# Kernel tuning notes

Hardware: AMD Instinct MI355X
Metric: run time of the kernel (lower is better)

Reference implementation:

```python
import jax, jax.numpy as jnp
import numpy as np

C = 512      # filters
G = 32       # groups
EPS = 1e-6

def setup_inputs() -> dict:
    key = jax.random.key(0)
    ks = jax.random.split(key, 10)
    B, H, W = 2, 64, 64
    inputs = jax.random.normal(ks[0], (B, H, W, C), dtype=jnp.float32)
    scale = 1.0 / np.sqrt(C)
    def w(k):
        return jax.random.normal(k, (C, C), dtype=jnp.float32) * scale
    return {
        "inputs": inputs,
        "gn_gamma": jnp.ones((C,), jnp.float32),
        "gn_beta": jnp.zeros((C,), jnp.float32),
        "wq": w(ks[1]), "bq": jnp.zeros((C,), jnp.float32),
        "wk": w(ks[2]), "bk": jnp.zeros((C,), jnp.float32),
        "wv": w(ks[3]), "bv": jnp.zeros((C,), jnp.float32),
        "wo": w(ks[4]), "bo": jnp.zeros((C,), jnp.float32),
    }

def _group_norm(x, gamma, beta):
    B, H, W, c = x.shape
    xg = x.reshape(B, H, W, G, c // G)
    mean = jnp.mean(xg, axis=(1, 2, 4), keepdims=True)
    var = jnp.var(xg, axis=(1, 2, 4), keepdims=True)
    xg = (xg - mean) * jax.lax.rsqrt(var + EPS)
    return xg.reshape(B, H, W, c) * gamma + beta

def reference(inputs, gn_gamma, gn_beta, wq, bq, wk, bk, wv, bv, wo, bo):
    B, H, W, c = inputs.shape
    x = _group_norm(inputs, gn_gamma, gn_beta)
    # 1x1 convs == per-pixel linear layers
    q = (x @ wq + bq).reshape(B, H * W, c)
    k = (x @ wk + bk).reshape(B, H * W, c)
    v = (x @ wv + bv).reshape(B, H * W, c)
    q = q * jnp.asarray(1.0 / np.sqrt(float(c)), q.dtype)
    scores = jnp.einsum('bnc,bmc->bnm', q, k).astype(jnp.float32)  # [B,N,N]
    probs = jax.nn.softmax(scores, axis=-1).astype(inputs.dtype)
    attn = jnp.einsum('bnm,bmc->bnc', probs, v)
    out = attn.reshape(B, H, W, c) @ wo + bo
    return out + inputs
```

## Files before the change

### kernel.cpp

```cpp
#include <hip/hip_runtime.h>
#include <math.h>

typedef __bf16 bf16;
typedef __bf16 bf16x8 __attribute__((ext_vector_type(8)));
typedef float  f32x4  __attribute__((ext_vector_type(4)));

#define DEV __device__ __forceinline__

DEV void gload_lds16(const bf16* g, bf16* l) {
  __builtin_amdgcn_global_load_lds(
      (const __attribute__((address_space(1))) void*)g,
      (__attribute__((address_space(3))) void*)l, 16, 0, 0);
}

#define OFF_STATS 0UL
#define OFF_XN    512UL
#define OFF_WTQKV 8389120UL
#define OFF_WOT   9961984UL
#define OFF_BIASQ 10486272UL
#define OFF_QKV   10492416UL
#define OFF_VT    35658240UL
#define OFF_S     44046848UL
#define OFF_ATTN  111155712UL

__global__ __launch_bounds__(256) void gn_part_k(const float* __restrict__ x,
                                                 float2* __restrict__ part) {
  const int blk = blockIdx.x;
  const int chunk = blk & 15;
  const int bg = blk >> 4;
  const int b = bg >> 5, g = bg & 31;
  const int t = threadIdx.x;
  const int p = chunk * 256 + t;
  const float* xp = x + (size_t)b * (4096 * 512) + (size_t)p * 512 + g * 16;
  float4 v0 = *(const float4*)(xp);
  float4 v1 = *(const float4*)(xp + 4);
  float4 v2 = *(const float4*)(xp + 8);
  float4 v3 = *(const float4*)(xp + 12);
  float s  = v0.x + v0.y + v0.z + v0.w + v1.x + v1.y + v1.z + v1.w
           + v2.x + v2.y + v2.z + v2.w + v3.x + v3.y + v3.z + v3.w;
  float ss = v0.x*v0.x + v0.y*v0.y + v0.z*v0.z + v0.w*v0.w
           + v1.x*v1.x + v1.y*v1.y + v1.z*v1.z + v1.w*v1.w
           + v2.x*v2.x + v2.y*v2.y + v2.z*v2.z + v2.w*v2.w
           + v3.x*v3.x + v3.y*v3.y + v3.z*v3.z + v3.w*v3.w;
#pragma unroll
  for (int off = 32; off; off >>= 1) {
    s  += __shfl_xor(s, off);
    ss += __shfl_xor(ss, off);
  }
  __shared__ float rs[4], rss[4];
  const int w = t >> 6, l = t & 63;
  if (l == 0) { rs[w] = s; rss[w] = ss; }
  __syncthreads();
  if (t == 0)
    part[blk] = make_float2(rs[0] + rs[1] + rs[2] + rs[3],
                            rss[0] + rss[1] + rss[2] + rss[3]);
}

__global__ void gn_finish_k(const float2* __restrict__ part,
                            float2* __restrict__ stats) {
  const int g = threadIdx.x;
  float s = 0.f, ss = 0.f;
#pragma unroll
  for (int c = 0; c < 16; ++c) {
    float2 p = part[g * 16 + c];
    s += p.x; ss += p.y;
  }
  float mean = s * (1.0f / 65536.0f);
  float var  = ss * (1.0f / 65536.0f) - mean * mean;
  stats[g] = make_float2(mean, 1.0f / sqrtf(var + 1e-6f));
}

__global__ __launch_bounds__(256) void gn_apply_k(const float* __restrict__ x,
                                                  const float2* __restrict__ stats,
                                                  const float* __restrict__ gamma,
                                                  const float* __restrict__ beta,
                                                  bf16* __restrict__ xn) {
  size_t i = ((size_t)blockIdx.x * 256 + threadIdx.x) * 8;
  const int c = (int)(i & 511);
  const int b = (int)(i >> 21);
  float2 st = stats[b * 32 + (c >> 4)];
  float4 xa = *(const float4*)(x + i);
  float4 xb = *(const float4*)(x + i + 4);
  float4 ga = *(const float4*)(gamma + c);
  float4 gb = *(const float4*)(gamma + c + 4);
  float4 ba = *(const float4*)(beta + c);
  float4 bb = *(const float4*)(beta + c + 4);
  bf16x8 o;
  o[0] = (bf16)((xa.x - st.x) * st.y * ga.x + ba.x);
  o[1] = (bf16)((xa.y - st.x) * st.y * ga.y + ba.y);
  o[2] = (bf16)((xa.z - st.x) * st.y * ga.z + ba.z);
  o[3] = (bf16)((xa.w - st.x) * st.y * ga.w + ba.w);
  o[4] = (bf16)((xb.x - st.x) * st.y * gb.x + bb.x);
  o[5] = (bf16)((xb.y - st.x) * st.y * gb.y + bb.y);
  o[6] = (bf16)((xb.z - st.x) * st.y * gb.z + bb.z);
  o[7] = (bf16)((xb.w - st.x) * st.y * gb.w + bb.w);
  *(bf16x8*)(xn + i) = o;
}

__global__ void prep_w_k(const float* __restrict__ wq, const float* __restrict__ wk,
                         const float* __restrict__ wv, const float* __restrict__ wo,
                         bf16* __restrict__ wt_qkv, bf16* __restrict__ wot, float qscale) {
  const int z = blockIdx.z;
  const float* W = (z == 0) ? wq : (z == 1) ? wk : (z == 2) ? wv : wo;
  bf16* dst = (z < 3) ? (wt_qkv + (size_t)z * 512 * 512) : wot;
  const float s = (z == 0) ? qscale : 1.0f;
  __shared__ float tile[32][33];
  const int i0 = blockIdx.y * 32;
  const int o0 = blockIdx.x * 32;
#pragma unroll
  for (int r = threadIdx.y; r < 32; r += 8)
    tile[r][threadIdx.x] = W[(size_t)(i0 + r) * 512 + o0 + threadIdx.x];
  __syncthreads();
#pragma unroll
  for (int r = threadIdx.y; r < 32; r += 8)
    dst[(size_t)(o0 + r) * 512 + i0 + threadIdx.x] = (bf16)(tile[threadIdx.x][r] * s);
}

__global__ void prep_bias_k(const float* __restrict__ bq, const float* __restrict__ bk,
                            const float* __restrict__ bv, float* __restrict__ bias_qkv,
                            float qscale) {
  int i = blockIdx.x * 256 + threadIdx.x;
  float v = (i < 512) ? bq[i] * qscale : (i < 1024) ? bk[i - 512] : bv[i - 1024];
  bias_qkv[i] = v;
}

__global__ void transpose_v_k(const bf16* __restrict__ qkv, bf16* __restrict__ vt) {
  __shared__ bf16 tile[32][33];
  const int z = blockIdx.z;
  const int n0 = blockIdx.x * 32, d0 = blockIdx.y * 32;
  const bf16* src = qkv + (size_t)z * 4096 * 1536 + 1024;
#pragma unroll
  for (int r = threadIdx.y; r < 32; r += 8)
    tile[r][threadIdx.x] = src[(size_t)(n0 + r) * 1536 + d0 + threadIdx.x];
  __syncthreads();
  bf16* dst = vt + (size_t)z * 512 * 4096;
#pragma unroll
  for (int r = threadIdx.y; r < 32; r += 8)
    dst[(size_t)(d0 + r) * 4096 + n0 + threadIdx.x] = tile[threadIdx.x][r];
}

__global__ __launch_bounds__(256) void softmax_k(bf16* __restrict__ S) {
  const int t = threadIdx.x;
  bf16* p = S + (size_t)blockIdx.x * 4096 + t * 16;
  bf16x8 u0 = *(const bf16x8*)p;
  bf16x8 u1 = *(const bf16x8*)(p + 8);
  float v[16];
#pragma unroll
  for (int j = 0; j < 8; ++j) { v[j] = (float)u0[j]; v[j + 8] = (float)u1[j]; }
  float m = v[0];
#pragma unroll
  for (int j = 1; j < 16; ++j) m = fmaxf(m, v[j]);
#pragma unroll
  for (int off = 32; off; off >>= 1) m = fmaxf(m, __shfl_xor(m, off));
  __shared__ float red[4];
  const int w = t >> 6, l = t & 63;
  if (l == 0) red[w] = m;
  __syncthreads();
  m = fmaxf(fmaxf(red[0], red[1]), fmaxf(red[2], red[3]));
  __syncthreads();
  float s = 0.f;
#pragma unroll
  for (int j = 0; j < 16; ++j) { v[j] = __expf(v[j] - m); s += v[j]; }
#pragma unroll
  for (int off = 32; off; off >>= 1) s += __shfl_xor(s, off);
  if (l == 0) red[w] = s;
  __syncthreads();
  s = red[0] + red[1] + red[2] + red[3];
  const float inv = 1.0f / s;
#pragma unroll
  for (int j = 0; j < 8; ++j) { u0[j] = (bf16)(v[j] * inv); u1[j] = (bf16)(v[j + 8] * inv); }
  *(bf16x8*)p = u0;
  *(bf16x8*)(p + 8) = u1;
}

template <int BM, int BN, int EPI, int GX, int GY, int GZ>
__global__ __launch_bounds__(256, 2) void gemm_nt(
    const bf16* __restrict__ A, int lda, long sAz,
    const bf16* __restrict__ B, int ldb, long sBz,
    void* __restrict__ C, int ldc, long sCz,
    int nk,
    const float* __restrict__ bias,
    const float* __restrict__ resid) {
  constexpr int WM = BM / 2, WN = BN / 2;
  constexpr int FM = BM / 32, FN = BN / 32;
  constexpr int NWG = GX * GY * GZ;
  constexpr int CPX = NWG / 8;
  __shared__ alignas(16) bf16 As[2][BM * 64];
  __shared__ alignas(16) bf16 Bs[2][BN * 64];

  const int lin = blockIdx.x;
  const int wid = (lin & 7) * CPX + (lin >> 3);
  const int bx = wid % GX;
  const int by = (wid / GX) % GY;
  const int bz = wid / (GX * GY);

  const int t = threadIdx.x;
  const bf16* Aq = A + (size_t)bz * sAz + (size_t)by * BM * lda;
  const bf16* Bq = B + (size_t)bz * sBz + (size_t)bx * BN * ldb;

  const int srow = t >> 3;
  const int sg   = (t & 7) ^ (srow & 7);

  auto stage = [&](int buf, int kt) {
    const int k0 = kt * 64 + sg * 8;
#pragma unroll
    for (int i = 0; i < BM / 32; ++i)
      gload_lds16(Aq + (size_t)(i * 32 + srow) * lda + k0, &As[buf][i * 2048 + t * 8]);
#pragma unroll
    for (int i = 0; i < BN / 32; ++i)
      gload_lds16(Bq + (size_t)(i * 32 + srow) * ldb + k0, &Bs[buf][i * 2048 + t * 8]);
  };

  const int l = t & 63, w = t >> 6;
  const int wr = w >> 1, wc = w & 1;
  const int lr = l & 15, kh = l >> 4;
  const int rs = lr & 7;

  f32x4 acc[FM][FN] = {};

  stage(0, 0);
  for (int kt = 0; kt < nk; ++kt) {
    __syncthreads();
    if (kt + 1 < nk) stage((kt + 1) & 1, kt + 1);
    const int buf = kt & 1;
    bf16x8 a[2][FM], b[2][FN];
#pragma unroll
    for (int h = 0; h < 2; ++h) {
      const int g = ((h * 4 + kh) ^ rs) * 8;
#pragma unroll
      for (int m = 0; m < FM; ++m)
        a[h][m] = *(const bf16x8*)(&As[buf][(wr * WM + m * 16 + lr) * 64 + g]);
#pragma unroll
      for (int n = 0; n < FN; ++n)
        b[h][n] = *(const bf16x8*)(&Bs[buf][(wc * WN + n * 16 + lr) * 64 + g]);
    }
#pragma unroll
    for (int h = 0; h < 2; ++h)
#pragma unroll
      for (int m = 0; m < FM; ++m)
#pragma unroll
        for (int n = 0; n < FN; ++n)
          acc[m][n] = __builtin_amdgcn_mfma_f32_16x16x32_bf16(a[h][m], b[h][n], acc[m][n], 0, 0, 0);
  }

  const int gr0 = by * BM + wr * WM + kh * 4;
  const int gc0 = bx * BN + wc * WN + lr;
#pragma unroll
  for (int m = 0; m < FM; ++m)
#pragma unroll
    for (int n = 0; n < FN; ++n) {
      const int c = gc0 + n * 16;
      float bv = 0.f;
      if constexpr (EPI >= 1) bv = bias[c];
#pragma unroll
      for (int j = 0; j < 4; ++j) {
        const int r = gr0 + m * 16 + j;
        float val = acc[m][n][j] + bv;
        if constexpr (EPI == 2) {
          float* Cf = (float*)C + (size_t)bz * sCz;
          Cf[(size_t)r * ldc + c] = val + resid[(size_t)r * ldc + c];
        } else {
          bf16* Cb = (bf16*)C + (size_t)bz * sCz;
          Cb[(size_t)r * ldc + c] = (bf16)val;
        }
      }
    }
}

extern "C" void kernel_launch(void* const* d_in, const int* in_sizes, int n_in,
                              void* d_out, int out_size, void* d_ws, size_t ws_size,
                              hipStream_t stream) {
  const float* x     = (const float*)d_in[0];
  const float* gamma = (const float*)d_in[1];
  const float* beta  = (const float*)d_in[2];
  const float* wq = (const float*)d_in[3];
  const float* bq = (const float*)d_in[4];
  const float* wk = (const float*)d_in[5];
  const float* bk = (const float*)d_in[6];
  const float* wv = (const float*)d_in[7];
  const float* bv = (const float*)d_in[8];
  const float* wo = (const float*)d_in[9];
  const float* bo = (const float*)d_in[10];
  float* out = (float*)d_out;
  char* ws = (char*)d_ws;

  float2* stats    = (float2*)(ws + OFF_STATS);
  bf16*   xn       = (bf16*)(ws + OFF_XN);
  bf16*   wt_qkv   = (bf16*)(ws + OFF_WTQKV);
  bf16*   wot      = (bf16*)(ws + OFF_WOT);
  float*  bias_qkv = (float*)(ws + OFF_BIASQ);
  bf16*   qkv      = (bf16*)(ws + OFF_QKV);
  bf16*   vt       = (bf16*)(ws + OFF_VT);
  bf16*   S        = (bf16*)(ws + OFF_S);
  bf16*   attn     = (bf16*)(ws + OFF_ATTN);
  float2* gn_part  = (float2*)(ws + OFF_S);

  const float qscale = 0.04419417382415922f;

  prep_w_k<<<dim3(16, 16, 4), dim3(32, 8), 0, stream>>>(wq, wk, wv, wo, wt_qkv, wot, qscale);
  prep_bias_k<<<6, 256, 0, stream>>>(bq, bk, bv, bias_qkv, qscale);
  gn_part_k<<<1024, 256, 0, stream>>>(x, gn_part);
  gn_finish_k<<<1, 64, 0, stream>>>(gn_part, stats);
  gn_apply_k<<<2048, 256, 0, stream>>>(x, stats, gamma, beta, xn);

  gemm_nt<128, 128, 1, 12, 64, 1><<<768, 256, 0, stream>>>(
      xn, 512, 0, wt_qkv, 512, 0, qkv, 1536, 0, 512 / 64, bias_qkv, nullptr);

  gemm_nt<128, 128, 0, 32, 32, 2><<<2048, 256, 0, stream>>>(
      qkv, 1536, 4096L * 1536, qkv + 512, 1536, 4096L * 1536,
      S, 4096, 4096L * 4096, 512 / 64, nullptr, nullptr);

  softmax_k<<<8192, 256, 0, stream>>>(S);

  transpose_v_k<<<dim3(128, 16, 2), dim3(32, 8), 0, stream>>>(qkv, vt);

  gemm_nt<128, 64, 0, 8, 32, 2><<<512, 256, 0, stream>>>(
      S, 4096, 4096L * 4096, vt, 4096, 512L * 4096,
      attn, 512, 4096L * 512, 4096 / 64, nullptr, nullptr);

  gemm_nt<64, 128, 2, 4, 128, 1><<<512, 256, 0, stream>>>(
      attn, 512, 0, wot, 512, 0, out, 512, 0, 512 / 64, bo, x);
}
```

Measured before the change: 185.4 us.

## Add triple-buffered GEMM with fine-grained vmcnt waits for the P@V stage

Introduces a gemm_deep kernel that keeps three LDS stages in flight, issuing each load two iterations ahead. It waits with explicit s_waitcnt vmcnt counts instead of draining all loads, and raises wave priority around the MFMA block. It is used for the long-K (4096) probs×V GEMM to hide global-load latency behind compute. The cost is more LDS per block, which may limit occupancy, and hardcoded vmcnt literals that only hold when each stage issues six loads.

```diff
diff --git a/kernel.cpp b/kernel.cpp
--- a/kernel.cpp
+++ b/kernel.cpp
@@ -6,6 +6,8 @@
 typedef float  f32x4  __attribute__((ext_vector_type(4)));
 
 #define DEV __device__ __forceinline__
+#define VMCNT(n) asm volatile("s_waitcnt vmcnt(" #n ")" ::: "memory")
+#define CFENCE  asm volatile("" ::: "memory")
 
 DEV void gload_lds16(const bf16* g, bf16* l) {
   __builtin_amdgcn_global_load_lds(
@@ -267,6 +269,115 @@
     }
 }
 
+template <int BM, int BN, int EPI, int GX, int GY, int GZ>
+__global__ __launch_bounds__(256, 2) void gemm_deep(
+    const bf16* __restrict__ A, int lda, long sAz,
+    const bf16* __restrict__ B, int ldb, long sBz,
+    void* __restrict__ C, int ldc, long sCz,
+    int ns,
+    const float* __restrict__ bias,
+    const float* __restrict__ resid) {
+  constexpr int WM = BM / 2, WN = BN / 2;
+  constexpr int FM = BM / 32, FN = BN / 32;
+  constexpr int L = BM / 32 + BN / 32;
+  static_assert(L == 6, "vmcnt literals below assume L==6");
+  constexpr int NWG = GX * GY * GZ;
+  constexpr int CPX = NWG / 8;
+  __shared__ alignas(16) bf16 As[3][BM * 64];
+  __shared__ alignas(16) bf16 Bs[3][BN * 64];
+
+  const int lin = blockIdx.x;
+  const int wid = (lin & 7) * CPX + (lin >> 3);
+  const int bx = wid % GX;
+  const int by = (wid / GX) % GY;
+  const int bz = wid / (GX * GY);
+
+  const int t = threadIdx.x;
+  const bf16* Aq = A + (size_t)bz * sAz + (size_t)by * BM * lda;
+  const bf16* Bq = B + (size_t)bz * sBz + (size_t)bx * BN * ldb;
+
+  const int srow = t >> 3;
+  const int sg   = (t & 7) ^ (srow & 7);
+
+  auto stage = [&](int ss) {
+    const int buf = ss % 3;
+    const int k0 = ss * 64 + sg * 8;
+#pragma unroll
+    for (int i = 0; i < BM / 32; ++i)
+      gload_lds16(Aq + (size_t)(i * 32 + srow) * lda + k0, &As[buf][i * 2048 + t * 8]);
+#pragma unroll
+    for (int i = 0; i < BN / 32; ++i)
+      gload_lds16(Bq + (size_t)(i * 32 + srow) * ldb + k0, &Bs[buf][i * 2048 + t * 8]);
+  };
+
+  const int l = t & 63, w = t >> 6;
+  const int wr = w >> 1, wc = w & 1;
+  const int lr = l & 15, kh = l >> 4;
+  const int rs = lr & 7;
+
+  f32x4 acc[FM][FN] = {};
+
+  stage(0);
+  if (1 < ns) stage(1);
+
+  for (int s = 0; s < ns; ++s) {
+    if (s + 2 < ns) stage(s + 2);
+    CFENCE;
+    const int ahead = ns - 1 - s;
+    if (ahead >= 2)      VMCNT(12);
+    else if (ahead == 1) VMCNT(6);
+    else                 VMCNT(0);
+    __builtin_amdgcn_s_barrier();
+    CFENCE;
+    const int buf = s % 3;
+    bf16x8 a[2][FM], b[2][FN];
+#pragma unroll
+    for (int h = 0; h < 2; ++h) {
+      const int g = ((h * 4 + kh) ^ rs) * 8;
+#pragma unroll
+      for (int m = 0; m < FM; ++m)
+        a[h][m] = *(const bf16x8*)(&As[buf][(wr * WM + m * 16 + lr) * 64 + g]);
+#pragma unroll
+      for (int n = 0; n < FN; ++n)
+        b[h][n] = *(const bf16x8*)(&Bs[buf][(wc * WN + n * 16 + lr) * 64 + g]);
+    }
+    __builtin_amdgcn_s_setprio(1);
+#pragma unroll
+    for (int h = 0; h < 2; ++h)
+#pragma unroll
+      for (int m = 0; m < FM; ++m)
+#pragma unroll
+        for (int n = 0; n < FN; ++n)
+          acc[m][n] = __builtin_amdgcn_mfma_f32_16x16x32_bf16(a[h][m], b[h][n], acc[m][n], 0, 0, 0);
+    __builtin_amdgcn_s_setprio(0);
+    CFENCE;
+    __builtin_amdgcn_s_barrier();
+  }
+
+  const int gr0 = by * BM + wr * WM + kh * 4;
+  const int gc0 = bx * BN + wc * WN + lr;
+#pragma unroll
+  for (int m = 0; m < FM; ++m)
+#pragma unroll
+    for (int n = 0; n < FN; ++n) {
+      const int c = gc0 + n * 16;
+      float bv = 0.f;
+      if constexpr (EPI >= 1) bv = bias[c];
+#pragma unroll
+      for (int j = 0; j < 4; ++j) {
+        const int r = gr0 + m * 16 + j;
+        float val = acc[m][n][j] + bv;
+        if constexpr (EPI == 2) {
+          float* Cf = (float*)C + (size_t)bz * sCz;
+          Cf[(size_t)r * ldc + c] = val + resid[(size_t)r * ldc + c];
+        } else {
+          bf16* Cb = (bf16*)C + (size_t)bz * sCz;
+          Cb[(size_t)r * ldc + c] = (bf16)val;
+        }
+      }
+    }
+}
+
 extern "C" void kernel_launch(void* const* d_in, const int* in_sizes, int n_in,
                               void* d_out, int out_size, void* d_ws, size_t ws_size,
                               hipStream_t stream) {
@@ -314,7 +425,7 @@
 
   transpose_v_k<<<dim3(128, 16, 2), dim3(32, 8), 0, stream>>>(qkv, vt);
 
-  gemm_nt<128, 64, 0, 8, 32, 2><<<512, 256, 0, stream>>>(
+  gemm_deep<128, 64, 0, 8, 32, 2><<<512, 256, 0, stream>>>(
       S, 4096, 4096L * 4096, vt, 4096, 512L * 4096,
       attn, 512, 4096L * 512, 4096 / 64, nullptr, nullptr);
 
```

New measurement: 186.7 us. About the same (+0.7%).

## Add 8-wave 256-tile ping-pong GEMM for QK and split-K PV

Applied to the files above, without the earlier changes.

Introduces a 512-thread GEMM kernel with 256-row tiles, double-buffered LDS staging interleaved with MFMA quarter-blocks under explicit barriers and vmcnt waits. It is used for the QK^T score GEMM and for the PV GEMM, which is now split along K into two fp32 partial outputs that a new reduce kernel sums into bf16. The workspace layout is rearranged to fit the partial buffers. The aim is higher MFMA utilisation through larger tiles and overlap of global-to-LDS loads with compute, and more parallelism for the PV GEMM. The cost is extra fp32 partial traffic, an additional kernel launch and hand-tuned wait counts that must match the number of loads issued.

```diff
diff --git a/kernel.cpp b/kernel.cpp
--- a/kernel.cpp
+++ b/kernel.cpp
@@ -6,6 +6,9 @@
 typedef float  f32x4  __attribute__((ext_vector_type(4)));
 
 #define DEV __device__ __forceinline__
+#define VMCNT(n) asm volatile("s_waitcnt vmcnt(" #n ")" ::: "memory")
+#define CFENCE  asm volatile("" ::: "memory")
+#define BAR()   { CFENCE; __builtin_amdgcn_s_barrier(); CFENCE; }
 
 DEV void gload_lds16(const bf16* g, bf16* l) {
   __builtin_amdgcn_global_load_lds(
@@ -14,14 +17,17 @@
 }
 
 #define OFF_STATS 0UL
-#define OFF_XN    512UL
-#define OFF_WTQKV 8389120UL
-#define OFF_WOT   9961984UL
-#define OFF_BIASQ 10486272UL
-#define OFF_QKV   10492416UL
-#define OFF_VT    35658240UL
-#define OFF_S     44046848UL
-#define OFF_ATTN  111155712UL
+#define OFF_WOT   1024UL
+#define OFF_BIASQ 525312UL
+#define OFF_WTQKV 531456UL
+#define OFF_XN    2104320UL
+#define OFF_QKV   10492928UL
+#define OFF_VT    35658752UL
+#define OFF_S     44047360UL
+#define OFF_P0    2104320UL
+#define OFF_P1    18881536UL
+#define OFF_ATTN  44047360UL
+#define OFF_GNP   44047360UL
 
 __global__ __launch_bounds__(256) void gn_part_k(const float* __restrict__ x,
                                                  float2* __restrict__ part) {
@@ -173,6 +179,22 @@
   *(bf16x8*)(p + 8) = u1;
 }
 
+__global__ __launch_bounds__(256) void reduce_pv_k(const float* __restrict__ p0,
+                                                   const float* __restrict__ p1,
+                                                   bf16* __restrict__ attn) {
+  size_t i = ((size_t)blockIdx.x * 256 + threadIdx.x) * 8;
+  float4 a = *(const float4*)(p0 + i);
+  float4 b = *(const float4*)(p0 + i + 4);
+  float4 c = *(const float4*)(p1 + i);
+  float4 d = *(const float4*)(p1 + i + 4);
+  bf16x8 o;
+  o[0] = (bf16)(a.x + c.x); o[1] = (bf16)(a.y + c.y);
+  o[2] = (bf16)(a.z + c.z); o[3] = (bf16)(a.w + c.w);
+  o[4] = (bf16)(b.x + d.x); o[5] = (bf16)(b.y + d.y);
+  o[6] = (bf16)(b.z + d.z); o[7] = (bf16)(b.w + d.w);
+  *(bf16x8*)(attn + i) = o;
+}
+
 template <int BM, int BN, int EPI, int GX, int GY, int GZ>
 __global__ __launch_bounds__(256, 2) void gemm_nt(
     const bf16* __restrict__ A, int lda, long sAz,
@@ -262,6 +284,166 @@
         } else {
           bf16* Cb = (bf16*)C + (size_t)bz * sCz;
           Cb[(size_t)r * ldc + c] = (bf16)val;
+        }
+      }
+    }
+}
+
+template <int BM, int BN, int WR, int WC, int EPI, int GX, int GY, int GZ, int KS>
+__global__ __launch_bounds__(512, 2) void gemm_8p(
+    const bf16* __restrict__ A, int lda, long sAz,
+    const bf16* __restrict__ B, int ldb, long sBz,
+    void* __restrict__ C0, void* __restrict__ C1, int ldc, long sCz,
+    int nt) {
+  constexpr int WM = BM / WR, WN = BN / WC;
+  constexpr int FM = WM / 16, FN = WN / 16;
+  constexpr int HM = FM / 2, HN = FN / 2;
+  constexpr int LA = BM / 128, LB = BN / 128;
+  constexpr int NWG = GX * KS * GY * GZ;
+  constexpr int CPX = NWG / 8;
+  static_assert(WR * WC == 8, "8 waves");
+  static_assert(LA == 2 && (LB == 1 || LB == 2), "vmcnt literals");
+
+  __shared__ alignas(16) bf16 As[2][BM * 64];
+  __shared__ alignas(16) bf16 Bs[2][BN * 64];
+
+  const int t = threadIdx.x;
+  const int lin = blockIdx.x;
+  const int wid = (lin & 7) * CPX + (lin >> 3);
+  const int bx = wid % GX;
+  const int ks = (wid / GX) % KS;
+  const int by = (wid / (GX * KS)) % GY;
+  const int bz = wid / (GX * KS * GY);
+
+  const long kOff = (long)ks * nt * 64;
+  const bf16* Aq = A + (size_t)bz * sAz + (size_t)by * BM * lda + kOff;
+  const bf16* Bq = B + (size_t)bz * sBz + (size_t)bx * BN * ldb + kOff;
+
+  const int srow = t >> 3;
+  const int sgr  = (t & 7) ^ (srow & 7);
+
+  auto stageA = [&](int buf, int tile, int half) {
+    const bf16* src = Aq + (size_t)(half * (BM / 2) + srow) * lda + tile * 64 + sgr * 8;
+    bf16* dst = &As[buf][(half * (BM / 2)) * 64] + t * 8;
+#pragma unroll
+    for (int j = 0; j < LA; ++j)
+      gload_lds16(src + (size_t)(j * 64) * lda, dst + j * 4096);
+  };
+  auto stageB = [&](int buf, int tile, int half) {
+    const bf16* src = Bq + (size_t)(half * (BN / 2) + srow) * ldb + tile * 64 + sgr * 8;
+    bf16* dst = &Bs[buf][(half * (BN / 2)) * 64] + t * 8;
+#pragma unroll
+    for (int j = 0; j < LB; ++j)
+      gload_lds16(src + (size_t)(j * 64) * ldb, dst + j * 4096);
+  };
+
+  const int l = t & 63, w = t >> 6;
+  const int wr = w / WC, wc = w % WC;
+  const int lr = l & 15, kh = l >> 4;
+  const int rs8 = lr & 7;
+
+  bf16x8 af[HM][2], bf_[HN][2];
+  auto readA = [&](int buf, int qm) {
+#pragma unroll
+    for (int i = 0; i < HM; ++i)
+#pragma unroll
+      for (int h = 0; h < 2; ++h)
+        af[i][h] = *(const bf16x8*)(
+            &As[buf][(wr * WM + qm * (WM / 2) + i * 16 + lr) * 64 + (((h * 4 + kh) ^ rs8) * 8)]);
+  };
+  auto readB = [&](int buf, int qn) {
+#pragma unroll
+    for (int j = 0; j < HN; ++j)
+#pragma unroll
+      for (int h = 0; h < 2; ++h)
+        bf_[j][h] = *(const bf16x8*)(
+            &Bs[buf][(wc * WN + qn * (WN / 2) + j * 16 + lr) * 64 + (((h * 4 + kh) ^ rs8) * 8)]);
+  };
+
+  f32x4 acc[FM][FN] = {};
+
+#define MFMAQ(QM, QN) { \
+  __builtin_amdgcn_s_setprio(1); \
+  _Pragma("unroll") for (int ii = 0; ii < HM; ++ii) \
+  _Pragma("unroll") for (int jj = 0; jj < HN; ++jj) \
+  _Pragma("unroll") for (int h = 0; h < 2; ++h) \
+    acc[(QM)*HM + ii][(QN)*HN + jj] = __builtin_amdgcn_mfma_f32_16x16x32_bf16( \
+        af[ii][h], bf_[jj][h], acc[(QM)*HM + ii][(QN)*HN + jj], 0, 0, 0); \
+  __builtin_amdgcn_s_setprio(0); }
+#define WAIT_LB() { if constexpr (LB == 1) VMCNT(1); else VMCNT(2); }
+
+  stageA(0, 0, 0); stageA(0, 0, 1); stageB(0, 0, 0); stageB(0, 0, 1);
+  WAIT_LB();
+  BAR();
+
+  const int half = nt >> 1;
+  for (int i = 0; i < half; ++i) {
+    const int t1 = 2 * i + 1, t2 = 2 * i + 2;
+    const bool last = (i == half - 1);
+    readA(0, 0); readB(0, 0);
+    stageA(1, t1, 0);
+    BAR();
+    MFMAQ(0, 0);
+    BAR();
+    readA(0, 1);
+    stageA(1, t1, 1);
+    BAR();
+    MFMAQ(1, 0);
+    VMCNT(4);
+    BAR();
+    readB(0, 1);
+    stageB(1, t1, 0);
+    BAR();
+    MFMAQ(1, 1);
+    BAR();
+    readA(0, 0);
+    stageB(1, t1, 1);
+    BAR();
+    MFMAQ(0, 1);
+    WAIT_LB();
+    BAR();
+    readA(1, 0); readB(1, 0);
+    if (!last) stageA(0, t2, 0);
+    BAR();
+    MFMAQ(0, 0);
+    BAR();
+    readA(1, 1);
+    if (!last) stageA(0, t2, 1);
+    BAR();
+    MFMAQ(1, 0);
+    if (last) { VMCNT(0); } else { VMCNT(4); }
+    BAR();
+    readB(1, 1);
+    if (!last) stageB(0, t2, 0);
+    BAR();
+    MFMAQ(1, 1);
+    BAR();
+    readA(1, 0);
+    if (!last) stageB(0, t2, 1);
+    BAR();
+    MFMAQ(0, 1);
+    WAIT_LB();
+    BAR();
+  }
+#undef MFMAQ
+#undef WAIT_LB
+
+  const int gr0 = by * BM + wr * WM + kh * 4;
+  const int gc0 = bx * BN + wc * WN + lr;
+#pragma unroll
+  for (int m = 0; m < FM; ++m)
+#pragma unroll
+    for (int n = 0; n < FN; ++n) {
+      const int c = gc0 + n * 16;
+#pragma unroll
+      for (int j = 0; j < 4; ++j) {
+        const int r = gr0 + m * 16 + j;
+        if constexpr (EPI == 0) {
+          bf16* Cb = (bf16*)C0 + (size_t)bz * sCz;
+          Cb[(size_t)r * ldc + c] = (bf16)acc[m][n][j];
+        } else {
+          float* Cf = (float*)(ks ? C1 : C0) + (size_t)bz * sCz;
+          Cf[(size_t)r * ldc + c] = acc[m][n][j];
         }
       }
     }
@@ -285,15 +467,17 @@
   char* ws = (char*)d_ws;
 
   float2* stats    = (float2*)(ws + OFF_STATS);
-  bf16*   xn       = (bf16*)(ws + OFF_XN);
-  bf16*   wt_qkv   = (bf16*)(ws + OFF_WTQKV);
   bf16*   wot      = (bf16*)(ws + OFF_WOT);
   float*  bias_qkv = (float*)(ws + OFF_BIASQ);
+  bf16*   wt_qkv   = (bf16*)(ws + OFF_WTQKV);
+  bf16*   xn       = (bf16*)(ws + OFF_XN);
   bf16*   qkv      = (bf16*)(ws + OFF_QKV);
   bf16*   vt       = (bf16*)(ws + OFF_VT);
   bf16*   S        = (bf16*)(ws + OFF_S);
+  float*  p0       = (float*)(ws + OFF_P0);
+  float*  p1       = (float*)(ws + OFF_P1);
   bf16*   attn     = (bf16*)(ws + OFF_ATTN);
-  float2* gn_part  = (float2*)(ws + OFF_S);
+  float2* gn_part  = (float2*)(ws + OFF_GNP);
 
   const float qscale = 0.04419417382415922f;
 
@@ -306,17 +490,19 @@
   gemm_nt<128, 128, 1, 12, 64, 1><<<768, 256, 0, stream>>>(
       xn, 512, 0, wt_qkv, 512, 0, qkv, 1536, 0, 512 / 64, bias_qkv, nullptr);
 
-  gemm_nt<128, 128, 0, 32, 32, 2><<<2048, 256, 0, stream>>>(
+  gemm_8p<256, 256, 2, 4, 0, 16, 16, 2, 1><<<512, 512, 0, stream>>>(
       qkv, 1536, 4096L * 1536, qkv + 512, 1536, 4096L * 1536,
-      S, 4096, 4096L * 4096, 512 / 64, nullptr, nullptr);
+      S, nullptr, 4096, 4096L * 4096, 512 / 64);
 
   softmax_k<<<8192, 256, 0, stream>>>(S);
 
   transpose_v_k<<<dim3(128, 16, 2), dim3(32, 8), 0, stream>>>(qkv, vt);
 
-  gemm_nt<128, 64, 0, 8, 32, 2><<<512, 256, 0, stream>>>(
+  gemm_8p<256, 128, 4, 2, 3, 4, 16, 2, 2><<<256, 512, 0, stream>>>(
       S, 4096, 4096L * 4096, vt, 4096, 512L * 4096,
-      attn, 512, 4096L * 512, 4096 / 64, nullptr, nullptr);
+      p0, p1, 512, 4096L * 512, 2048 / 64);
+
+  reduce_pv_k<<<2048, 256, 0, stream>>>(p0, p1, attn);
 
   gemm_nt<64, 128, 2, 4, 128, 1><<<512, 256, 0, stream>>>(
       attn, 512, 0, wot, 512, 0, out, 512, 0, 512 / 64, bo, x);
```

After: 176.5 us, median of 2. 1.05x faster.

## Fuse exp into QK GEMM, defer softmax normalization, write V transposed

Applied to the files above, without the earlier changes.

The QK^T GEMM epilogue now writes exp(score) directly, without subtracting the row max. A light rowsum kernel computes 1/rowsum, and the PV GEMM epilogue applies it, replacing the separate read-modify-write softmax pass over S. The V projection is split into its own GEMM whose epilogue stores V already transposed, so the standalone transpose kernel goes away. The workspace layout is reshuffled to match. Dropping max subtraction risks overflow if scores exceed the exp range, which this input distribution is unlikely to reach.

```diff
diff --git a/kernel.cpp b/kernel.cpp
--- a/kernel.cpp
+++ b/kernel.cpp
@@ -2,6 +2,7 @@
 #include <math.h>
 
 typedef __bf16 bf16;
+typedef __bf16 bf16x4 __attribute__((ext_vector_type(4)));
 typedef __bf16 bf16x8 __attribute__((ext_vector_type(8)));
 typedef float  f32x4  __attribute__((ext_vector_type(4)));
 
@@ -14,14 +15,16 @@
 }
 
 #define OFF_STATS 0UL
-#define OFF_XN    512UL
-#define OFF_WTQKV 8389120UL
-#define OFF_WOT   9961984UL
-#define OFF_BIASQ 10486272UL
-#define OFF_QKV   10492416UL
-#define OFF_VT    35658240UL
-#define OFF_S     44046848UL
-#define OFF_ATTN  111155712UL
+#define OFF_WOT   1024UL
+#define OFF_BIASQ 525312UL
+#define OFF_WTQKV 531456UL
+#define OFF_XN    2104320UL
+#define OFF_QK    10492928UL
+#define OFF_VT    35658752UL
+#define OFF_S     44047360UL
+#define OFF_INVL  111156224UL
+#define OFF_ATTN  2104320UL
+#define OFF_GNP   44047360UL
 
 __global__ __launch_bounds__(256) void gn_part_k(const float* __restrict__ x,
                                                  float2* __restrict__ part) {
@@ -124,53 +127,23 @@
   bias_qkv[i] = v;
 }
 
-__global__ void transpose_v_k(const bf16* __restrict__ qkv, bf16* __restrict__ vt) {
-  __shared__ bf16 tile[32][33];
-  const int z = blockIdx.z;
-  const int n0 = blockIdx.x * 32, d0 = blockIdx.y * 32;
-  const bf16* src = qkv + (size_t)z * 4096 * 1536 + 1024;
-#pragma unroll
-  for (int r = threadIdx.y; r < 32; r += 8)
-    tile[r][threadIdx.x] = src[(size_t)(n0 + r) * 1536 + d0 + threadIdx.x];
-  __syncthreads();
-  bf16* dst = vt + (size_t)z * 512 * 4096;
-#pragma unroll
-  for (int r = threadIdx.y; r < 32; r += 8)
-    dst[(size_t)(d0 + r) * 4096 + n0 + threadIdx.x] = tile[threadIdx.x][r];
-}
-
-__global__ __launch_bounds__(256) void softmax_k(bf16* __restrict__ S) {
-  const int t = threadIdx.x;
-  bf16* p = S + (size_t)blockIdx.x * 4096 + t * 16;
+__global__ __launch_bounds__(256) void rowsum_k(const bf16* __restrict__ S,
+                                                float* __restrict__ invl) {
+  const int r = blockIdx.x;
+  const bf16* p = S + (size_t)r * 4096 + threadIdx.x * 16;
   bf16x8 u0 = *(const bf16x8*)p;
   bf16x8 u1 = *(const bf16x8*)(p + 8);
-  float v[16];
-#pragma unroll
-  for (int j = 0; j < 8; ++j) { v[j] = (float)u0[j]; v[j + 8] = (float)u1[j]; }
-  float m = v[0];
-#pragma unroll
-  for (int j = 1; j < 16; ++j) m = fmaxf(m, v[j]);
-#pragma unroll
-  for (int off = 32; off; off >>= 1) m = fmaxf(m, __shfl_xor(m, off));
+  float s = 0.f;
+#pragma unroll
+  for (int j = 0; j < 8; ++j) s += (float)u0[j] + (float)u1[j];
+#pragma unroll
+  for (int off = 32; off; off >>= 1) s += __shfl_xor(s, off);
   __shared__ float red[4];
-  const int w = t >> 6, l = t & 63;
-  if (l == 0) red[w] = m;
-  __syncthreads();
-  m = fmaxf(fmaxf(red[0], red[1]), fmaxf(red[2], red[3]));
-  __syncthreads();
-  float s = 0.f;
-#pragma unroll
-  for (int j = 0; j < 16; ++j) { v[j] = __expf(v[j] - m); s += v[j]; }
-#pragma unroll
-  for (int off = 32; off; off >>= 1) s += __shfl_xor(s, off);
+  const int w = threadIdx.x >> 6, l = threadIdx.x & 63;
   if (l == 0) red[w] = s;
   __syncthreads();
-  s = red[0] + red[1] + red[2] + red[3];
-  const float inv = 1.0f / s;
-#pragma unroll
-  for (int j = 0; j < 8; ++j) { u0[j] = (bf16)(v[j] * inv); u1[j] = (bf16)(v[j + 8] * inv); }
-  *(bf16x8*)p = u0;
-  *(bf16x8*)(p + 8) = u1;
+  if (threadIdx.x == 0)
+    invl[r] = 1.0f / (red[0] + red[1] + red[2] + red[3]);
 }
 
 template <int BM, int BN, int EPI, int GX, int GY, int GZ>
@@ -250,18 +223,41 @@
 #pragma unroll
     for (int n = 0; n < FN; ++n) {
       const int c = gc0 + n * 16;
-      float bv = 0.f;
-      if constexpr (EPI >= 1) bv = bias[c];
-#pragma unroll
-      for (int j = 0; j < 4; ++j) {
-        const int r = gr0 + m * 16 + j;
-        float val = acc[m][n][j] + bv;
-        if constexpr (EPI == 2) {
-          float* Cf = (float*)C + (size_t)bz * sCz;
-          Cf[(size_t)r * ldc + c] = val + resid[(size_t)r * ldc + c];
-        } else {
-          bf16* Cb = (bf16*)C + (size_t)bz * sCz;
-          Cb[(size_t)r * ldc + c] = (bf16)val;
+      if constexpr (EPI == 7) {
+        const int r0 = gr0 + m * 16;
+        const int z = r0 >> 12, nn = r0 & 4095;
+        const float bv = bias[c];
+        bf16x4 v;
+#pragma unroll
+        for (int j = 0; j < 4; ++j) v[j] = (bf16)(acc[m][n][j] + bv);
+        *(bf16x4*)((bf16*)C + (size_t)z * (512 * 4096) + (size_t)c * 4096 + nn) = v;
+      } else if constexpr (EPI == 8) {
+        bf16* Cb = (bf16*)C + (size_t)bz * sCz;
+#pragma unroll
+        for (int j = 0; j < 4; ++j) {
+          const int r = gr0 + m * 16 + j;
+          Cb[(size_t)r * ldc + c] = (bf16)__expf(acc[m][n][j]);
+        }
+      } else if constexpr (EPI == 5) {
+        bf16* Cb = (bf16*)C + (size_t)bz * sCz;
+#pragma unroll
+        for (int j = 0; j < 4; ++j) {
+          const int r = gr0 + m * 16 + j;
+          Cb[(size_t)r * ldc + c] = (bf16)(acc[m][n][j] * bias[bz * 4096 + r]);
+        }
+      } else {
+        const float bv = bias[c];
+#pragma unroll
+        for (int j = 0; j < 4; ++j) {
+          const int r = gr0 + m * 16 + j;
+          float val = acc[m][n][j] + bv;
+          if constexpr (EPI == 2) {
+            float* Cf = (float*)C + (size_t)bz * sCz;
+            Cf[(size_t)r * ldc + c] = val + resid[(size_t)r * ldc + c];
+          } else {
+            bf16* Cb = (bf16*)C + (size_t)bz * sCz;
+            Cb[(size_t)r * ldc + c] = (bf16)val;
+          }
         }
       }
     }
@@ -285,15 +281,16 @@
   char* ws = (char*)d_ws;
 
   float2* stats    = (float2*)(ws + OFF_STATS);
-  bf16*   xn       = (bf16*)(ws + OFF_XN);
-  bf16*   wt_qkv   = (bf16*)(ws + OFF_WTQKV);
   bf16*   wot      = (bf16*)(ws + OFF_WOT);
   float*  bias_qkv = (float*)(ws + OFF_BIASQ);
-  bf16*   qkv      = (bf16*)(ws + OFF_QKV);
+  bf16*   wt_qkv   = (bf16*)(ws + OFF_WTQKV);
+  bf16*   xn       = (bf16*)(ws + OFF_XN);
+  bf16*   qk       = (bf16*)(ws + OFF_QK);
   bf16*   vt       = (bf16*)(ws + OFF_VT);
   bf16*   S        = (bf16*)(ws + OFF_S);
+  float*  invl     = (float*)(ws + OFF_INVL);
   bf16*   attn     = (bf16*)(ws + OFF_ATTN);
-  float2* gn_part  = (float2*)(ws + OFF_S);
+  float2* gn_part  = (float2*)(ws + OFF_GNP);
 
   const float qscale = 0.04419417382415922f;
 
@@ -303,20 +300,22 @@
   gn_finish_k<<<1, 64, 0, stream>>>(gn_part, stats);
   gn_apply_k<<<2048, 256, 0, stream>>>(x, stats, gamma, beta, xn);
 
-  gemm_nt<128, 128, 1, 12, 64, 1><<<768, 256, 0, stream>>>(
-      xn, 512, 0, wt_qkv, 512, 0, qkv, 1536, 0, 512 / 64, bias_qkv, nullptr);
-
-  gemm_nt<128, 128, 0, 32, 32, 2><<<2048, 256, 0, stream>>>(
-      qkv, 1536, 4096L * 1536, qkv + 512, 1536, 4096L * 1536,
+  gemm_nt<128, 128, 1, 8, 64, 1><<<512, 256, 0, stream>>>(
+      xn, 512, 0, wt_qkv, 512, 0, qk, 1024, 0, 512 / 64, bias_qkv, nullptr);
+
+  gemm_nt<128, 128, 7, 4, 64, 1><<<256, 256, 0, stream>>>(
+      xn, 512, 0, wt_qkv + 1024 * 512, 512, 0, vt, 0, 0, 512 / 64,
+      bias_qkv + 1024, nullptr);
+
+  gemm_nt<128, 128, 8, 32, 32, 2><<<2048, 256, 0, stream>>>(
+      qk, 1024, 4096L * 1024, qk + 512, 1024, 4096L * 1024,
       S, 4096, 4096L * 4096, 512 / 64, nullptr, nullptr);
 
-  softmax_k<<<8192, 256, 0, stream>>>(S);
-
-  transpose_v_k<<<dim3(128, 16, 2), dim3(32, 8), 0, stream>>>(qkv, vt);
-
-  gemm_nt<128, 64, 0, 8, 32, 2><<<512, 256, 0, stream>>>(
+  rowsum_k<<<8192, 256, 0, stream>>>(S, invl);
+
+  gemm_nt<128, 64, 5, 8, 32, 2><<<512, 256, 0, stream>>>(
       S, 4096, 4096L * 4096, vt, 4096, 512L * 4096,
-      attn, 512, 4096L * 512, 4096 / 64, nullptr, nullptr);
+      attn, 512, 4096L * 512, 4096 / 64, invl, nullptr);
 
   gemm_nt<64, 128, 2, 4, 128, 1><<<512, 256, 0, stream>>>(
       attn, 512, 0, wot, 512, 0, out, 512, 0, 512 / 64, bo, x);
```

New measurement: 172.4 us. 1.08x faster.
